# Kernel tuning notes

Hardware: AMD Instinct MI355X
Metric: run time of the kernel (lower is better)

The kernel has to match this reference:

```python
import jax, jax.numpy as jnp
import numpy as np

LEFT, RIGHT = 64, 64  # left_size, right_size; hidden = LEFT*RIGHT = 4096


def _cayley(raw):
    """torch nn.utils.parametrizations.orthogonal(..., orthogonal_map='cayley',
    use_trivialization=False): A = triu(raw, 1); X = A - A^T (skew-symmetric);
    Q = (I - X/2)^{-1} (I + X/2)."""
    n = raw.shape[0]
    A = jnp.triu(raw, 1)
    X = A - A.T
    Id = jnp.eye(n, dtype=raw.dtype)
    return jnp.linalg.solve(Id - 0.5 * X, Id + 0.5 * X)


def setup_inputs() -> dict:
    key = jax.random.key(0)
    ks = jax.random.split(key, 8)
    B, S = 4, 2048
    H = LEFT * RIGHT
    inp = jax.random.normal(ks[0], (B, S, H), dtype=jnp.float32)
    raw_u_left = jax.random.normal(ks[1], (LEFT, LEFT), dtype=jnp.float32) * 0.02
    raw_v_left = jax.random.normal(ks[2], (LEFT, LEFT), dtype=jnp.float32) * 0.02
    raw_u_right = jax.random.normal(ks[3], (RIGHT, RIGHT), dtype=jnp.float32) * 0.02
    raw_v_right = jax.random.normal(ks[4], (RIGHT, RIGHT), dtype=jnp.float32) * 0.02
    diag_left = jnp.ones((LEFT,), dtype=jnp.float32)
    diag_right = jnp.ones((RIGHT,), dtype=jnp.float32)
    diag_scale = jnp.ones((H,), dtype=jnp.float32) + 0.01 * jax.random.normal(ks[5], (H,), dtype=jnp.float32)
    return {
        "inp": inp,
        "raw_u_left": raw_u_left,
        "raw_v_left": raw_v_left,
        "diag_left": diag_left,
        "raw_u_right": raw_u_right,
        "raw_v_right": raw_v_right,
        "diag_right": diag_right,
        "diag_scale": diag_scale,
        "inv_t": 0,
    }


def reference(inp, raw_u_left, raw_v_left, diag_left, raw_u_right, raw_v_right,
              diag_right, diag_scale, inv_t):
    # add_diag=True, use_diag=True path
    if inv_t:
        x = inp / diag_scale
        dl = 1.0 / diag_left
        dr = 1.0 / diag_right
    else:
        x = inp * diag_scale
        dl = diag_left
        dr = diag_right
    # Cayley-parametrized orthogonal factors
    Ul = _cayley(raw_u_left)
    Vl = _cayley(raw_v_left)
    Ur = _cayley(raw_u_right)
    Vr = _cayley(raw_v_right)
    # SVD-style reconstruction: M = U @ diag(d) @ V^T
    ML = (Ul * dl[None, :]) @ Vl.T  # [LEFT, LEFT]
    MR = (Ur * dr[None, :]) @ Vr.T  # [RIGHT, RIGHT]
    # Kronecker matmul: view last dim as [LEFT, RIGHT], out = ML^T @ X @ MR
    orig_shape = x.shape
    xb = x.reshape(-1, LEFT, RIGHT)  # [B*S, LEFT, RIGHT]
    out = jnp.einsum('bij,ik,jl->bkl', xb, ML, MR)
    return out.reshape(orig_shape)
```

## Files before the change

### kernel.cpp

```cpp
#include <hip/hip_runtime.h>
#include <hip/hip_bf16.h>

typedef short short8 __attribute__((ext_vector_type(8)));
typedef short short4v __attribute__((ext_vector_type(4)));
typedef float f32x4 __attribute__((ext_vector_type(4)));

#define HID 4096
#define CST 68

__device__ __forceinline__ unsigned short f2bf(float f) {
    unsigned int u = __float_as_uint(f);
    u = (u + 0x7FFFu + ((u >> 16) & 1u)) >> 16;
    return (unsigned short)u;
}

__device__ __forceinline__ void mm_acc(f32x4 acc[4], const float* SA, const float* SB,
                                       int i, int j0) {
    f32x4 z = {0.f, 0.f, 0.f, 0.f};
    acc[0] = z; acc[1] = z; acc[2] = z; acc[3] = z;
#pragma unroll 4
    for (int k = 0; k < 64; ++k) {
        float a = SA[i * CST + k];
        const f32x4* bp = reinterpret_cast<const f32x4*>(SB + k * CST + j0);
        acc[0] += a * bp[0];
        acc[1] += a * bp[1];
        acc[2] += a * bp[2];
        acc[3] += a * bp[3];
    }
}

__global__ __launch_bounds__(256) void cayley_build_kernel(
    const float* __restrict__ rul, const float* __restrict__ rvl, const float* __restrict__ dl,
    const float* __restrict__ rur, const float* __restrict__ rvr, const float* __restrict__ dr,
    const int* __restrict__ invt,
    unsigned short* __restrict__ plb, unsigned short* __restrict__ mrtb)
{
    __shared__ __align__(16) float Yu[64 * CST], Au[64 * CST], Pu[64 * CST];
    __shared__ __align__(16) float Yv[64 * CST], Av[64 * CST], Pv[64 * CST];
    __shared__ float dd[64];

    const float* ru; const float* rv; const float* dv; unsigned short* ob;
    if (blockIdx.x == 0) { ru = rul; rv = rvl; dv = dl; ob = plb; }
    else                 { ru = rur; rv = rvr; dv = dr; ob = mrtb; }

    const int tid = threadIdx.x;
    const int i = tid >> 2;
    const int j0 = (tid & 3) << 4;

#pragma unroll
    for (int q = 0; q < 16; ++q) {
        int j = j0 + q;
        float vu = 0.f, vv = 0.f;
        if (j > i)      { vu =  ru[i * 64 + j]; vv =  rv[i * 64 + j]; }
        else if (j < i) { vu = -ru[j * 64 + i]; vv = -rv[j * 64 + i]; }
        Yu[i * CST + j] = 0.5f * vu;
        Yv[i * CST + j] = 0.5f * vv;
    }
    if (tid < 64) { float d = dv[tid]; dd[tid] = (invt[0] != 0) ? (1.0f / d) : d; }
    __syncthreads();

    f32x4 au[4], av[4];

    mm_acc(au, Yu, Yu, i, j0); mm_acc(av, Yv, Yv, i, j0);
    __syncthreads();
#pragma unroll
    for (int q = 0; q < 4; ++q) {
        *reinterpret_cast<f32x4*>(Au + i * CST + j0 + 4 * q) = au[q];
        *reinterpret_cast<f32x4*>(Av + i * CST + j0 + 4 * q) = av[q];
    }
    __syncthreads();
#pragma unroll
    for (int q = 0; q < 4; ++q) {
        *reinterpret_cast<f32x4*>(Pu + i * CST + j0 + 4 * q) =
            *reinterpret_cast<const f32x4*>(Yu + i * CST + j0 + 4 * q) +
            *reinterpret_cast<const f32x4*>(Au + i * CST + j0 + 4 * q);
        *reinterpret_cast<f32x4*>(Pv + i * CST + j0 + 4 * q) =
            *reinterpret_cast<const f32x4*>(Yv + i * CST + j0 + 4 * q) +
            *reinterpret_cast<const f32x4*>(Av + i * CST + j0 + 4 * q);
    }
    __syncthreads();
    mm_acc(au, Pu, Au, i, j0); mm_acc(av, Pv, Av, i, j0);
    __syncthreads();
#pragma unroll
    for (int q = 0; q < 4; ++q) {
        *reinterpret_cast<f32x4*>(Pu + i * CST + j0 + 4 * q) += au[q];
        *reinterpret_cast<f32x4*>(Pv + i * CST + j0 + 4 * q) += av[q];
    }
    __syncthreads();
    mm_acc(au, Au, Au, i, j0); mm_acc(av, Av, Av, i, j0);
    __syncthreads();
#pragma unroll
    for (int q = 0; q < 4; ++q) {
        *reinterpret_cast<f32x4*>(Au + i * CST + j0 + 4 * q) = au[q];
        *reinterpret_cast<f32x4*>(Av + i * CST + j0 + 4 * q) = av[q];
    }
    __syncthreads();
    mm_acc(au, Pu, Au, i, j0); mm_acc(av, Pv, Av, i, j0);
    __syncthreads();
#pragma unroll
    for (int q = 0; q < 4; ++q) {
        *reinterpret_cast<f32x4*>(Pu + i * CST + j0 + 4 * q) += au[q];
        *reinterpret_cast<f32x4*>(Pv + i * CST + j0 + 4 * q) += av[q];
    }
    __syncthreads();

#pragma unroll
    for (int q = 0; q < 16; ++q) {
        int j = j0 + q;
        float idv = (i == j) ? 1.f : 0.f;
        Au[i * CST + j] = idv + 2.f * Pu[i * CST + j];
        Av[j * CST + i] = idv + 2.f * Pv[i * CST + j];
    }
    __syncthreads();

    f32x4 m[4];
    {
        f32x4 z = {0.f, 0.f, 0.f, 0.f};
        m[0] = z; m[1] = z; m[2] = z; m[3] = z;
    }
#pragma unroll 4
    for (int j = 0; j < 64; ++j) {
        float a = Au[i * CST + j] * dd[j];
        const f32x4* bp = reinterpret_cast<const f32x4*>(Av + j * CST + j0);
        m[0] += a * bp[0]; m[1] += a * bp[1]; m[2] += a * bp[2]; m[3] += a * bp[3];
    }
#pragma unroll
    for (int q = 0; q < 16; ++q)
        ob[(j0 + q) * 64 + i] = f2bf(m[q >> 2][q & 3]);
}

__global__ __launch_bounds__(256, 2) void kron_kernel(
    const float* __restrict__ inp, const float* __restrict__ ds,
    const unsigned short* __restrict__ plb, const unsigned short* __restrict__ mrtb,
    const int* __restrict__ invt, float* __restrict__ out, int ntok)
{
    __shared__ __align__(16) unsigned short zbuf[4][64 * 72];
    const int w = threadIdx.x >> 6;
    const int lane = threadIdx.x & 63;
    const int l15 = lane & 15;
    const int lg = lane >> 4;
    unsigned short* Zt = zbuf[w];
    const int rowoff = l15 * 64 + lg * 8;

    short8 bmr[2][4], apl[4][2];
#pragma unroll
    for (int tc = 0; tc < 4; ++tc)
#pragma unroll
        for (int s = 0; s < 2; ++s)
            bmr[s][tc] = *reinterpret_cast<const short8*>(
                mrtb + (tc * 16 + l15) * 64 + s * 32 + lg * 8);
#pragma unroll
    for (int tr = 0; tr < 4; ++tr)
#pragma unroll
        for (int s = 0; s < 2; ++s)
            apl[tr][s] = *reinterpret_cast<const short8*>(
                plb + (tr * 16 + l15) * 64 + s * 32 + lg * 8);

    const bool inv = (invt[0] != 0);
    f32x4 dsv[4][2][2];
#pragma unroll
    for (int tr = 0; tr < 4; ++tr)
#pragma unroll
        for (int s = 0; s < 2; ++s) {
            f32x4 d0 = *reinterpret_cast<const f32x4*>(ds + tr * 1024 + rowoff + s * 32);
            f32x4 d1 = *reinterpret_cast<const f32x4*>(ds + tr * 1024 + rowoff + s * 32 + 4);
            if (inv) {
#pragma unroll
                for (int e = 0; e < 4; ++e) { d0[e] = 1.0f / d0[e]; d1[e] = 1.0f / d1[e]; }
            }
            dsv[tr][s][0] = d0; dsv[tr][s][1] = d1;
        }

    const int t0 = blockIdx.x * 16 + w * 4;
    for (int it = 0; it < 4; ++it) {
        const int t = t0 + it;
        if (t >= ntok) return;
        const float* xt = inp + (size_t)t * HID;

        f32x4 acc[4][4];
        {
            f32x4 z = {0.f, 0.f, 0.f, 0.f};
#pragma unroll
            for (int a = 0; a < 4; ++a)
#pragma unroll
                for (int b = 0; b < 4; ++b) acc[a][b] = z;
        }
#pragma unroll
        for (int tr = 0; tr < 4; ++tr) {
            short8 a1[2];
#pragma unroll
            for (int s = 0; s < 2; ++s) {
                f32x4 x0 = *reinterpret_cast<const f32x4*>(xt + tr * 1024 + rowoff + s * 32);
                f32x4 x1 = *reinterpret_cast<const f32x4*>(xt + tr * 1024 + rowoff + s * 32 + 4);
                x0 *= dsv[tr][s][0];
                x1 *= dsv[tr][s][1];
                short8 f;
#pragma unroll
                for (int e = 0; e < 4; ++e) {
                    f[e]     = (short)f2bf(x0[e]);
                    f[e + 4] = (short)f2bf(x1[e]);
                }
                a1[s] = f;
            }
#pragma unroll
            for (int tc = 0; tc < 4; ++tc) {
                acc[tr][tc] = __builtin_amdgcn_mfma_f32_16x16x32_bf16(a1[0], bmr[0][tc], acc[tr][tc], 0, 0, 0);
                acc[tr][tc] = __builtin_amdgcn_mfma_f32_16x16x32_bf16(a1[1], bmr[1][tc], acc[tr][tc], 0, 0, 0);
            }
        }

#pragma unroll
        for (int tc = 0; tc < 4; ++tc)
#pragma unroll
            for (int tr = 0; tr < 4; ++tr) {
                short4v zz;
#pragma unroll
                for (int r = 0; r < 4; ++r) zz[r] = (short)f2bf(acc[tr][tc][r]);
                *reinterpret_cast<short4v*>(Zt + (tc * 16 + l15) * 72 + tr * 16 + lg * 4) = zz;
            }

        f32x4 y[4][4];
        {
            f32x4 z = {0.f, 0.f, 0.f, 0.f};
#pragma unroll
            for (int a = 0; a < 4; ++a)
#pragma unroll
                for (int b = 0; b < 4; ++b) y[a][b] = z;
        }
#pragma unroll
        for (int tc = 0; tc < 4; ++tc) {
            short8 b0 = *reinterpret_cast<const short8*>(Zt + (tc * 16 + l15) * 72 + lg * 8);
            short8 b1 = *reinterpret_cast<const short8*>(Zt + (tc * 16 + l15) * 72 + 32 + lg * 8);
#pragma unroll
            for (int tr = 0; tr < 4; ++tr) {
                y[tr][tc] = __builtin_amdgcn_mfma_f32_16x16x32_bf16(apl[tr][0], b0, y[tr][tc], 0, 0, 0);
                y[tr][tc] = __builtin_amdgcn_mfma_f32_16x16x32_bf16(apl[tr][1], b1, y[tr][tc], 0, 0, 0);
            }
        }

        float* op = out + (size_t)t * HID + (lg * 4) * 64 + l15;
#pragma unroll
        for (int tr = 0; tr < 4; ++tr)
#pragma unroll
            for (int tc = 0; tc < 4; ++tc)
#pragma unroll
                for (int r = 0; r < 4; ++r)
                    op[tr * 1024 + r * 64 + tc * 16] = y[tr][tc][r];
    }
}

extern "C" void kernel_launch(void* const* d_in, const int* in_sizes, int n_in,
                              void* d_out, int out_size, void* d_ws, size_t ws_size,
                              hipStream_t stream) {
    const float* inp = (const float*)d_in[0];
    const float* rul = (const float*)d_in[1];
    const float* rvl = (const float*)d_in[2];
    const float* dl  = (const float*)d_in[3];
    const float* rur = (const float*)d_in[4];
    const float* rvr = (const float*)d_in[5];
    const float* dr  = (const float*)d_in[6];
    const float* ds  = (const float*)d_in[7];
    const int*   invt = (const int*)d_in[8];
    float* out = (float*)d_out;

    unsigned short* plb  = (unsigned short*)d_ws;
    unsigned short* mrtb = plb + 4096;

    const int ntok = in_sizes[0] / HID;

    hipLaunchKernelGGL(cayley_build_kernel, dim3(2), dim3(256), 0, stream,
                       rul, rvl, dl, rur, rvr, dr, invt, plb, mrtb);
    const int nblk = (ntok + 15) / 16;
    hipLaunchKernelGGL(kron_kernel, dim3(nblk), dim3(256), 0, stream,
                       inp, ds, plb, mrtb, invt, out, ntok);
}
```

Baseline: 96.56 us.

## Restructure Cayley build to 1024 threads and vectorize kron output stores

The Cayley build kernel moves to 1024 threads per block, with each thread computing 4 outputs, and the U and V factors are processed one after the other to cut shared memory. In the kron kernel the second matmul is reoriented so results leave as contiguous f32x4 nontemporal stores instead of scalar strided stores. Its diag_scale registers are dropped in favour of per-iteration loads, tokens per block are halved, and the launch-bounds occupancy hint is removed. These changes target store coalescing, register pressure and the serial latency of the small build kernel, at the cost of repeated diag_scale loads and sequential U/V passes.

```diff
diff --git a/kernel.cpp b/kernel.cpp
--- a/kernel.cpp
+++ b/kernel.cpp
@@ -14,29 +14,24 @@
     return (unsigned short)u;
 }
 
-__device__ __forceinline__ void mm_acc(f32x4 acc[4], const float* SA, const float* SB,
-                                       int i, int j0) {
-    f32x4 z = {0.f, 0.f, 0.f, 0.f};
-    acc[0] = z; acc[1] = z; acc[2] = z; acc[3] = z;
-#pragma unroll 4
+__device__ __forceinline__ f32x4 mm4(const float* SA, const float* SB, int i, int j0) {
+    f32x4 acc = {0.f, 0.f, 0.f, 0.f};
+#pragma unroll 8
     for (int k = 0; k < 64; ++k) {
         float a = SA[i * CST + k];
-        const f32x4* bp = reinterpret_cast<const f32x4*>(SB + k * CST + j0);
-        acc[0] += a * bp[0];
-        acc[1] += a * bp[1];
-        acc[2] += a * bp[2];
-        acc[3] += a * bp[3];
-    }
-}
-
-__global__ __launch_bounds__(256) void cayley_build_kernel(
+        acc += a * *reinterpret_cast<const f32x4*>(SB + k * CST + j0);
+    }
+    return acc;
+}
+
+__global__ __launch_bounds__(1024) void cayley_build_kernel(
     const float* __restrict__ rul, const float* __restrict__ rvl, const float* __restrict__ dl,
     const float* __restrict__ rur, const float* __restrict__ rvr, const float* __restrict__ dr,
     const int* __restrict__ invt,
     unsigned short* __restrict__ plb, unsigned short* __restrict__ mrtb)
 {
-    __shared__ __align__(16) float Yu[64 * CST], Au[64 * CST], Pu[64 * CST];
-    __shared__ __align__(16) float Yv[64 * CST], Av[64 * CST], Pv[64 * CST];
+    __shared__ __align__(16) float Yw[64 * CST], Aw[64 * CST], Pw[64 * CST];
+    __shared__ __align__(16) float Qw[64 * CST], QTw[64 * CST];
     __shared__ float dd[64];
 
     const float* ru; const float* rv; const float* dv; unsigned short* ob;
@@ -44,92 +39,61 @@
     else                 { ru = rur; rv = rvr; dv = dr; ob = mrtb; }
 
     const int tid = threadIdx.x;
-    const int i = tid >> 2;
-    const int j0 = (tid & 3) << 4;
-
-#pragma unroll
-    for (int q = 0; q < 16; ++q) {
-        int j = j0 + q;
-        float vu = 0.f, vv = 0.f;
-        if (j > i)      { vu =  ru[i * 64 + j]; vv =  rv[i * 64 + j]; }
-        else if (j < i) { vu = -ru[j * 64 + i]; vv = -rv[j * 64 + i]; }
-        Yu[i * CST + j] = 0.5f * vu;
-        Yv[i * CST + j] = 0.5f * vv;
+    const int i = tid >> 4;
+    const int j0 = (tid & 15) << 2;
+
+    for (int pass = 0; pass < 2; ++pass) {
+        const float* raw = (pass == 0) ? ru : rv;
+#pragma unroll
+        for (int q = 0; q < 4; ++q) {
+            int j = j0 + q;
+            float v = 0.f;
+            if (j > i)      v =  raw[i * 64 + j];
+            else if (j < i) v = -raw[j * 64 + i];
+            Yw[i * CST + j] = 0.5f * v;
+        }
+        __syncthreads();
+        f32x4 a = mm4(Yw, Yw, i, j0);
+        __syncthreads();
+        *reinterpret_cast<f32x4*>(Aw + i * CST + j0) = a;
+        *reinterpret_cast<f32x4*>(Pw + i * CST + j0) =
+            a + *reinterpret_cast<const f32x4*>(Yw + i * CST + j0);
+        __syncthreads();
+        a = mm4(Pw, Aw, i, j0);
+        __syncthreads();
+        *reinterpret_cast<f32x4*>(Pw + i * CST + j0) += a;
+        __syncthreads();
+        a = mm4(Aw, Aw, i, j0);
+        __syncthreads();
+        *reinterpret_cast<f32x4*>(Aw + i * CST + j0) = a;
+        __syncthreads();
+        a = mm4(Pw, Aw, i, j0);
+        __syncthreads();
+        f32x4 p = *reinterpret_cast<const f32x4*>(Pw + i * CST + j0) + a;
+#pragma unroll
+        for (int q = 0; q < 4; ++q) {
+            int j = j0 + q;
+            float qv = ((i == j) ? 1.f : 0.f) + 2.f * p[q];
+            if (pass == 0) Qw[i * CST + j]  = qv;
+            else           QTw[j * CST + i] = qv;
+        }
+        __syncthreads();
     }
     if (tid < 64) { float d = dv[tid]; dd[tid] = (invt[0] != 0) ? (1.0f / d) : d; }
     __syncthreads();
 
-    f32x4 au[4], av[4];
-
-    mm_acc(au, Yu, Yu, i, j0); mm_acc(av, Yv, Yv, i, j0);
-    __syncthreads();
-#pragma unroll
-    for (int q = 0; q < 4; ++q) {
-        *reinterpret_cast<f32x4*>(Au + i * CST + j0 + 4 * q) = au[q];
-        *reinterpret_cast<f32x4*>(Av + i * CST + j0 + 4 * q) = av[q];
-    }
-    __syncthreads();
-#pragma unroll
-    for (int q = 0; q < 4; ++q) {
-        *reinterpret_cast<f32x4*>(Pu + i * CST + j0 + 4 * q) =
-            *reinterpret_cast<const f32x4*>(Yu + i * CST + j0 + 4 * q) +
-            *reinterpret_cast<const f32x4*>(Au + i * CST + j0 + 4 * q);
-        *reinterpret_cast<f32x4*>(Pv + i * CST + j0 + 4 * q) =
-            *reinterpret_cast<const f32x4*>(Yv + i * CST + j0 + 4 * q) +
-            *reinterpret_cast<const f32x4*>(Av + i * CST + j0 + 4 * q);
-    }
-    __syncthreads();
-    mm_acc(au, Pu, Au, i, j0); mm_acc(av, Pv, Av, i, j0);
-    __syncthreads();
-#pragma unroll
-    for (int q = 0; q < 4; ++q) {
-        *reinterpret_cast<f32x4*>(Pu + i * CST + j0 + 4 * q) += au[q];
-        *reinterpret_cast<f32x4*>(Pv + i * CST + j0 + 4 * q) += av[q];
-    }
-    __syncthreads();
-    mm_acc(au, Au, Au, i, j0); mm_acc(av, Av, Av, i, j0);
-    __syncthreads();
-#pragma unroll
-    for (int q = 0; q < 4; ++q) {
-        *reinterpret_cast<f32x4*>(Au + i * CST + j0 + 4 * q) = au[q];
-        *reinterpret_cast<f32x4*>(Av + i * CST + j0 + 4 * q) = av[q];
-    }
-    __syncthreads();
-    mm_acc(au, Pu, Au, i, j0); mm_acc(av, Pv, Av, i, j0);
-    __syncthreads();
-#pragma unroll
-    for (int q = 0; q < 4; ++q) {
-        *reinterpret_cast<f32x4*>(Pu + i * CST + j0 + 4 * q) += au[q];
-        *reinterpret_cast<f32x4*>(Pv + i * CST + j0 + 4 * q) += av[q];
-    }
-    __syncthreads();
-
-#pragma unroll
-    for (int q = 0; q < 16; ++q) {
-        int j = j0 + q;
-        float idv = (i == j) ? 1.f : 0.f;
-        Au[i * CST + j] = idv + 2.f * Pu[i * CST + j];
-        Av[j * CST + i] = idv + 2.f * Pv[i * CST + j];
-    }
-    __syncthreads();
-
-    f32x4 m[4];
-    {
-        f32x4 z = {0.f, 0.f, 0.f, 0.f};
-        m[0] = z; m[1] = z; m[2] = z; m[3] = z;
-    }
-#pragma unroll 4
+    f32x4 m = {0.f, 0.f, 0.f, 0.f};
+#pragma unroll 8
     for (int j = 0; j < 64; ++j) {
-        float a = Au[i * CST + j] * dd[j];
-        const f32x4* bp = reinterpret_cast<const f32x4*>(Av + j * CST + j0);
-        m[0] += a * bp[0]; m[1] += a * bp[1]; m[2] += a * bp[2]; m[3] += a * bp[3];
-    }
-#pragma unroll
-    for (int q = 0; q < 16; ++q)
-        ob[(j0 + q) * 64 + i] = f2bf(m[q >> 2][q & 3]);
-}
-
-__global__ __launch_bounds__(256, 2) void kron_kernel(
+        float aa = Qw[i * CST + j] * dd[j];
+        m += aa * *reinterpret_cast<const f32x4*>(QTw + j * CST + j0);
+    }
+#pragma unroll
+    for (int q = 0; q < 4; ++q)
+        ob[(j0 + q) * 64 + i] = f2bf(m[q]);
+}
+
+__global__ __launch_bounds__(256) void kron_kernel(
     const float* __restrict__ inp, const float* __restrict__ ds,
     const unsigned short* __restrict__ plb, const unsigned short* __restrict__ mrtb,
     const int* __restrict__ invt, float* __restrict__ out, int ntok)
@@ -142,39 +106,23 @@
     unsigned short* Zt = zbuf[w];
     const int rowoff = l15 * 64 + lg * 8;
 
-    short8 bmr[2][4], apl[4][2];
+    short8 bmr[2][4], bpl[2][4];
 #pragma unroll
     for (int tc = 0; tc < 4; ++tc)
 #pragma unroll
-        for (int s = 0; s < 2; ++s)
+        for (int s = 0; s < 2; ++s) {
             bmr[s][tc] = *reinterpret_cast<const short8*>(
                 mrtb + (tc * 16 + l15) * 64 + s * 32 + lg * 8);
-#pragma unroll
-    for (int tr = 0; tr < 4; ++tr)
-#pragma unroll
-        for (int s = 0; s < 2; ++s)
-            apl[tr][s] = *reinterpret_cast<const short8*>(
-                plb + (tr * 16 + l15) * 64 + s * 32 + lg * 8);
-
+            bpl[s][tc] = *reinterpret_cast<const short8*>(
+                plb + (tc * 16 + l15) * 64 + s * 32 + lg * 8);
+        }
     const bool inv = (invt[0] != 0);
-    f32x4 dsv[4][2][2];
-#pragma unroll
-    for (int tr = 0; tr < 4; ++tr)
-#pragma unroll
-        for (int s = 0; s < 2; ++s) {
-            f32x4 d0 = *reinterpret_cast<const f32x4*>(ds + tr * 1024 + rowoff + s * 32);
-            f32x4 d1 = *reinterpret_cast<const f32x4*>(ds + tr * 1024 + rowoff + s * 32 + 4);
-            if (inv) {
-#pragma unroll
-                for (int e = 0; e < 4; ++e) { d0[e] = 1.0f / d0[e]; d1[e] = 1.0f / d1[e]; }
-            }
-            dsv[tr][s][0] = d0; dsv[tr][s][1] = d1;
-        }
-
-    const int t0 = blockIdx.x * 16 + w * 4;
-    for (int it = 0; it < 4; ++it) {
+
+    const int t0 = (blockIdx.x * 4 + w) * 2;
+#pragma unroll
+    for (int it = 0; it < 2; ++it) {
         const int t = t0 + it;
-        if (t >= ntok) return;
+        if (t >= ntok) break;
         const float* xt = inp + (size_t)t * HID;
 
         f32x4 acc[4][4];
@@ -192,8 +140,14 @@
             for (int s = 0; s < 2; ++s) {
                 f32x4 x0 = *reinterpret_cast<const f32x4*>(xt + tr * 1024 + rowoff + s * 32);
                 f32x4 x1 = *reinterpret_cast<const f32x4*>(xt + tr * 1024 + rowoff + s * 32 + 4);
-                x0 *= dsv[tr][s][0];
-                x1 *= dsv[tr][s][1];
+                f32x4 d0 = *reinterpret_cast<const f32x4*>(ds + tr * 1024 + rowoff + s * 32);
+                f32x4 d1 = *reinterpret_cast<const f32x4*>(ds + tr * 1024 + rowoff + s * 32 + 4);
+                if (inv) {
+#pragma unroll
+                    for (int e = 0; e < 4; ++e) { x0[e] /= d0[e]; x1[e] /= d1[e]; }
+                } else {
+                    x0 *= d0; x1 *= d1;
+                }
                 short8 f;
 #pragma unroll
                 for (int e = 0; e < 4; ++e) {
@@ -219,33 +173,20 @@
                 *reinterpret_cast<short4v*>(Zt + (tc * 16 + l15) * 72 + tr * 16 + lg * 4) = zz;
             }
 
-        f32x4 y[4][4];
-        {
-            f32x4 z = {0.f, 0.f, 0.f, 0.f};
-#pragma unroll
-            for (int a = 0; a < 4; ++a)
-#pragma unroll
-                for (int b = 0; b < 4; ++b) y[a][b] = z;
-        }
-#pragma unroll
-        for (int tc = 0; tc < 4; ++tc) {
-            short8 b0 = *reinterpret_cast<const short8*>(Zt + (tc * 16 + l15) * 72 + lg * 8);
-            short8 b1 = *reinterpret_cast<const short8*>(Zt + (tc * 16 + l15) * 72 + 32 + lg * 8);
-#pragma unroll
-            for (int tr = 0; tr < 4; ++tr) {
-                y[tr][tc] = __builtin_amdgcn_mfma_f32_16x16x32_bf16(apl[tr][0], b0, y[tr][tc], 0, 0, 0);
-                y[tr][tc] = __builtin_amdgcn_mfma_f32_16x16x32_bf16(apl[tr][1], b1, y[tr][tc], 0, 0, 0);
-            }
-        }
-
-        float* op = out + (size_t)t * HID + (lg * 4) * 64 + l15;
-#pragma unroll
-        for (int tr = 0; tr < 4; ++tr)
-#pragma unroll
-            for (int tc = 0; tc < 4; ++tc)
-#pragma unroll
-                for (int r = 0; r < 4; ++r)
-                    op[tr * 1024 + r * 64 + tc * 16] = y[tr][tc][r];
+#pragma unroll
+        for (int trY = 0; trY < 4; ++trY) {
+            short8 a0 = *reinterpret_cast<const short8*>(Zt + (trY * 16 + l15) * 72 + lg * 8);
+            short8 a1 = *reinterpret_cast<const short8*>(Zt + (trY * 16 + l15) * 72 + 32 + lg * 8);
+#pragma unroll
+            for (int tcY = 0; tcY < 4; ++tcY) {
+                f32x4 y = {0.f, 0.f, 0.f, 0.f};
+                y = __builtin_amdgcn_mfma_f32_16x16x32_bf16(a0, bpl[0][tcY], y, 0, 0, 0);
+                y = __builtin_amdgcn_mfma_f32_16x16x32_bf16(a1, bpl[1][tcY], y, 0, 0, 0);
+                f32x4* dst = reinterpret_cast<f32x4*>(
+                    out + (size_t)t * HID + (tcY * 16 + l15) * 64 + trY * 16 + lg * 4);
+                __builtin_nontemporal_store(y, dst);
+            }
+        }
     }
 }
 
@@ -268,9 +209,9 @@
 
     const int ntok = in_sizes[0] / HID;
 
-    hipLaunchKernelGGL(cayley_build_kernel, dim3(2), dim3(256), 0, stream,
+    hipLaunchKernelGGL(cayley_build_kernel, dim3(2), dim3(1024), 0, stream,
                        rul, rvl, dl, rur, rvr, dr, invt, plb, mrtb);
-    const int nblk = (ntok + 15) / 16;
+    const int nblk = (ntok + 7) / 8;
     hipLaunchKernelGGL(kron_kernel, dim3(nblk), dim3(256), 0, stream,
                        inp, ds, plb, mrtb, invt, out, ntok);
 }
```

Measured after the change: 88.81 us. 1.09x faster.
